# Performance work log

Measured on AMD Instinct MI355X. Metric: run time of the kernel, lower is better.

## Reference

```python
import jax, jax.numpy as jnp
import numpy as np

N_NODES = 100000
D = 256
N_EDGES = 500000
N_CLASSES = 4


def setup_inputs() -> dict:
    key = jax.random.key(0)
    k1, k2, k3, k4 = jax.random.split(key, 4)
    inp = jax.random.normal(k1, (N_NODES, D), dtype=jnp.float32)
    r_indices = jax.random.randint(k2, (N_EDGES,), 0, N_NODES, dtype=jnp.int64)
    c_indices = jax.random.randint(k3, (N_EDGES,), 0, N_NODES, dtype=jnp.int64)
    # xavier-uniform-like init for the skinny classifier weight
    limit = float(np.sqrt(6.0 / (D + N_CLASSES)))
    weight = jax.random.uniform(k4, (D, N_CLASSES), dtype=jnp.float32,
                                minval=-limit, maxval=limit)
    return {"input": inp, "r_indices": r_indices, "c_indices": c_indices,
            "weight": weight}


def reference(input, r_indices, c_indices, weight):
    # dropout p=0.0 -> identity. Gather edge endpoints, abs diff, skinny matmul.
    diff = jnp.abs(input[r_indices] - input[c_indices])  # [E, D]
    out = jnp.einsum('ed,dc->ec', diff, weight)          # [E, C]
    return out
```

## Files before the change

kernel.cpp:

```cpp
#include <hip/hip_runtime.h>


#define NODES   100000
#define DIM     256
#define EDGES   500000
#define NCLS    4

__global__ __launch_bounds__(256) void quant_kernel(
    const float* __restrict__ in,
    unsigned char* __restrict__ tbl,
    float* __restrict__ scales)
{
    const int lane = threadIdx.x & 63;
    const int wid  = (blockIdx.x * blockDim.x + threadIdx.x) >> 6;
    const int n_waves = (gridDim.x * blockDim.x) >> 6;

    for (int row = wid; row < NODES; row += n_waves) {
        const float4 v = *(const float4*)(in + (size_t)row * DIM + lane * 4);
        float m = fmaxf(fmaxf(fabsf(v.x), fabsf(v.y)),
                        fmaxf(fabsf(v.z), fabsf(v.w)));
        #pragma unroll
        for (int s = 32; s >= 1; s >>= 1)
            m = fmaxf(m, __shfl_xor(m, s, 64));

        const float rs = (m > 0.f) ? 127.f / m : 0.f;
        uchar4 q;
        q.x = (unsigned char)__float2int_rn(fmaf(v.x, rs, 128.f));
        q.y = (unsigned char)__float2int_rn(fmaf(v.y, rs, 128.f));
        q.z = (unsigned char)__float2int_rn(fmaf(v.z, rs, 128.f));
        q.w = (unsigned char)__float2int_rn(fmaf(v.w, rs, 128.f));
        *(uchar4*)(tbl + (size_t)row * DIM + lane * 4) = q;

        if (lane == 0) scales[row] = (m > 0.f) ? m / 127.f : 0.f;
    }
}

__global__ __launch_bounds__(256, 6) void edge_mlp_i8_x2_kernel(
    const unsigned char* __restrict__ tbl,
    const float* __restrict__ scales,
    const int*   __restrict__ r_idx,
    const int*   __restrict__ c_idx,
    const float* __restrict__ weight,
    float*       __restrict__ out)
{
    const int lane = threadIdx.x & 63;
    const int half = lane >> 5;
    const int hl   = lane & 31;
    const int wid  = (blockIdx.x * blockDim.x + threadIdx.x) >> 6;
    const int n_waves = (gridDim.x * blockDim.x) >> 6;
    const int step = n_waves * 4;

    const int d0 = hl * 8;
    float4 w[8];
    #pragma unroll
    for (int j = 0; j < 8; ++j)
        w[j] = *(const float4*)(weight + (d0 + j) * NCLS);

    for (int e = wid * 4; e < EDGES; e += step) {
        const int eeA = e + half;
        const int eeB = e + 2 + half;

        const int rA = r_idx[eeA], cA = c_idx[eeA];
        const int rB = r_idx[eeB], cB = c_idx[eeB];

        const float srA = scales[rA], scA = scales[cA];
        const float srB = scales[rB], scB = scales[cB];
        const uint2 uaA = *(const uint2*)(tbl + (size_t)rA * DIM + d0);
        const uint2 ubA = *(const uint2*)(tbl + (size_t)cA * DIM + d0);
        const uint2 uaB = *(const uint2*)(tbl + (size_t)rB * DIM + d0);
        const uint2 ubB = *(const uint2*)(tbl + (size_t)cB * DIM + d0);

        float u, t;
        #define TERM(UA, UB, SH, W, SR, NSC, BB, ACC)                        \
            u = fmaf((float)((UA >> SH) & 0xffu), SR,                        \
                     fmaf((float)((UB >> SH) & 0xffu), NSC, BB));            \
            t = fabsf(u);                                                    \
            ACC.x = fmaf(t, W.x, ACC.x);                                     \
            ACC.y = fmaf(t, W.y, ACC.y);                                     \
            ACC.z = fmaf(t, W.z, ACC.z);                                     \
            ACC.w = fmaf(t, W.w, ACC.w);

        const float nscA = -scA;
        const float BA = 128.f * (scA - srA);
        float4 accA = make_float4(0.f, 0.f, 0.f, 0.f);
        TERM(uaA.x, ubA.x,  0, w[0], srA, nscA, BA, accA)
        TERM(uaA.x, ubA.x,  8, w[1], srA, nscA, BA, accA)
        TERM(uaA.x, ubA.x, 16, w[2], srA, nscA, BA, accA)
        TERM(uaA.x, ubA.x, 24, w[3], srA, nscA, BA, accA)
        TERM(uaA.y, ubA.y,  0, w[4], srA, nscA, BA, accA)
        TERM(uaA.y, ubA.y,  8, w[5], srA, nscA, BA, accA)
        TERM(uaA.y, ubA.y, 16, w[6], srA, nscA, BA, accA)
        TERM(uaA.y, ubA.y, 24, w[7], srA, nscA, BA, accA)

        const float nscB = -scB;
        const float BB = 128.f * (scB - srB);
        float4 accB = make_float4(0.f, 0.f, 0.f, 0.f);
        TERM(uaB.x, ubB.x,  0, w[0], srB, nscB, BB, accB)
        TERM(uaB.x, ubB.x,  8, w[1], srB, nscB, BB, accB)
        TERM(uaB.x, ubB.x, 16, w[2], srB, nscB, BB, accB)
        TERM(uaB.x, ubB.x, 24, w[3], srB, nscB, BB, accB)
        TERM(uaB.y, ubB.y,  0, w[4], srB, nscB, BB, accB)
        TERM(uaB.y, ubB.y,  8, w[5], srB, nscB, BB, accB)
        TERM(uaB.y, ubB.y, 16, w[6], srB, nscB, BB, accB)
        TERM(uaB.y, ubB.y, 24, w[7], srB, nscB, BB, accB)
        #undef TERM

        #pragma unroll
        for (int m = 16; m >= 1; m >>= 1) {
            accA.x += __shfl_xor(accA.x, m, 64);
            accB.x += __shfl_xor(accB.x, m, 64);
            accA.y += __shfl_xor(accA.y, m, 64);
            accB.y += __shfl_xor(accB.y, m, 64);
            accA.z += __shfl_xor(accA.z, m, 64);
            accB.z += __shfl_xor(accB.z, m, 64);
            accA.w += __shfl_xor(accA.w, m, 64);
            accB.w += __shfl_xor(accB.w, m, 64);
        }

        if (hl == 0) {
            *(float4*)(out + (size_t)eeA * NCLS) = accA;
            *(float4*)(out + (size_t)eeB * NCLS) = accB;
        }
    }
}

__global__ __launch_bounds__(256, 8) void edge_mlp_f32_kernel(
    const float* __restrict__ input,
    const int*   __restrict__ r_idx,
    const int*   __restrict__ c_idx,
    const float* __restrict__ weight,
    float*       __restrict__ out)
{
    const int lane = threadIdx.x & 63;
    const int wid  = (blockIdx.x * blockDim.x + threadIdx.x) >> 6;
    const int n_waves = (gridDim.x * blockDim.x) >> 6;

    const int d0 = lane * 4;
    const float4 w0 = *(const float4*)(weight + (d0 + 0) * NCLS);
    const float4 w1 = *(const float4*)(weight + (d0 + 1) * NCLS);
    const float4 w2 = *(const float4*)(weight + (d0 + 2) * NCLS);
    const float4 w3 = *(const float4*)(weight + (d0 + 3) * NCLS);

    for (int e = wid; e < EDGES; e += n_waves) {
        const int r = r_idx[e];
        const int c = c_idx[e];
        const float4 a = *(const float4*)(input + (size_t)r * DIM + d0);
        const float4 b = *(const float4*)(input + (size_t)c * DIM + d0);

        const float t0 = fabsf(a.x - b.x);
        const float t1 = fabsf(a.y - b.y);
        const float t2 = fabsf(a.z - b.z);
        const float t3 = fabsf(a.w - b.w);

        float4 acc;
        acc.x = t0 * w0.x + t1 * w1.x + t2 * w2.x + t3 * w3.x;
        acc.y = t0 * w0.y + t1 * w1.y + t2 * w2.y + t3 * w3.y;
        acc.z = t0 * w0.z + t1 * w1.z + t2 * w2.z + t3 * w3.z;
        acc.w = t0 * w0.w + t1 * w1.w + t2 * w2.w + t3 * w3.w;

        #pragma unroll
        for (int m = 32; m >= 1; m >>= 1) {
            acc.x += __shfl_xor(acc.x, m, 64);
            acc.y += __shfl_xor(acc.y, m, 64);
            acc.z += __shfl_xor(acc.z, m, 64);
            acc.w += __shfl_xor(acc.w, m, 64);
        }
        if (lane == 0) *(float4*)(out + (size_t)e * NCLS) = acc;
    }
}

extern "C" void kernel_launch(void* const* d_in, const int* in_sizes, int n_in,
                              void* d_out, int out_size, void* d_ws, size_t ws_size,
                              hipStream_t stream) {
    const float* input  = (const float*)d_in[0];
    const int*   r_idx  = (const int*)d_in[1];
    const int*   c_idx  = (const int*)d_in[2];
    const float* weight = (const float*)d_in[3];
    float* out = (float*)d_out;

    const size_t tbl_bytes   = (size_t)NODES * DIM;
    const size_t scale_bytes = (size_t)NODES * sizeof(float);

    if (ws_size >= tbl_bytes + scale_bytes) {
        unsigned char* tbl = (unsigned char*)d_ws;
        float* scales = (float*)((char*)d_ws + tbl_bytes);
        quant_kernel<<<2048, 256, 0, stream>>>(input, tbl, scales);
        edge_mlp_i8_x2_kernel<<<2048, 256, 0, stream>>>(tbl, scales, r_idx,
                                                        c_idx, weight, out);
    } else {
        edge_mlp_f32_kernel<<<2048, 256, 0, stream>>>(input, r_idx, c_idx,
                                                      weight, out);
    }
}
```

Measured before the change: 91.20 us.

## Precompute packed per-edge records of row offsets and scales before the gather

Adds a pass that packs each edge's row and column table offsets and their scales into a 16-byte record, so the main kernel does one vector load per edge instead of dependent index loads followed by scale gathers. This shortens the dependent-load chain ahead of the table gathers. In exchange it adds a kernel launch and writes then reads 8 MB of records, and it needs more workspace; if the workspace is too small, the old path runs instead.

```diff
diff --git a/kernel.cpp b/kernel.cpp
--- a/kernel.cpp
+++ b/kernel.cpp
@@ -35,11 +35,28 @@
     }
 }
 
-__global__ __launch_bounds__(256, 6) void edge_mlp_i8_x2_kernel(
-    const unsigned char* __restrict__ tbl,
-    const float* __restrict__ scales,
+__global__ __launch_bounds__(256) void rec_kernel(
     const int*   __restrict__ r_idx,
     const int*   __restrict__ c_idx,
+    const float* __restrict__ scales,
+    uint4*       __restrict__ recs)
+{
+    const int stride = gridDim.x * blockDim.x;
+    for (int e = blockIdx.x * blockDim.x + threadIdx.x; e < EDGES; e += stride) {
+        const int r = r_idx[e];
+        const int c = c_idx[e];
+        uint4 rec;
+        rec.x = (unsigned)r * DIM;
+        rec.y = (unsigned)c * DIM;
+        rec.z = __float_as_uint(scales[r]);
+        rec.w = __float_as_uint(scales[c]);
+        recs[e] = rec;
+    }
+}
+
+__global__ __launch_bounds__(256, 6) void edge_mlp_i8_rec_kernel(
+    const unsigned char* __restrict__ tbl,
+    const uint4* __restrict__ recs,
     const float* __restrict__ weight,
     float*       __restrict__ out)
 {
@@ -60,15 +77,18 @@
         const int eeA = e + half;
         const int eeB = e + 2 + half;
 
-        const int rA = r_idx[eeA], cA = c_idx[eeA];
-        const int rB = r_idx[eeB], cB = c_idx[eeB];
-
-        const float srA = scales[rA], scA = scales[cA];
-        const float srB = scales[rB], scB = scales[cB];
-        const uint2 uaA = *(const uint2*)(tbl + (size_t)rA * DIM + d0);
-        const uint2 ubA = *(const uint2*)(tbl + (size_t)cA * DIM + d0);
-        const uint2 uaB = *(const uint2*)(tbl + (size_t)rB * DIM + d0);
-        const uint2 ubB = *(const uint2*)(tbl + (size_t)cB * DIM + d0);
+        const uint4 recA = recs[eeA];
+        const uint4 recB = recs[eeB];
+
+        const float srA = __uint_as_float(recA.z);
+        const float scA = __uint_as_float(recA.w);
+        const float srB = __uint_as_float(recB.z);
+        const float scB = __uint_as_float(recB.w);
+
+        const uint2 uaA = *(const uint2*)(tbl + recA.x + d0);
+        const uint2 ubA = *(const uint2*)(tbl + recA.y + d0);
+        const uint2 uaB = *(const uint2*)(tbl + recB.x + d0);
+        const uint2 ubB = *(const uint2*)(tbl + recB.y + d0);
 
         float u, t;
         #define TERM(UA, UB, SH, W, SR, NSC, BB, ACC)                        \
@@ -124,6 +144,95 @@
     }
 }
 
+__global__ __launch_bounds__(256, 6) void edge_mlp_i8_x2_kernel(
+    const unsigned char* __restrict__ tbl,
+    const float* __restrict__ scales,
+    const int*   __restrict__ r_idx,
+    const int*   __restrict__ c_idx,
+    const float* __restrict__ weight,
+    float*       __restrict__ out)
+{
+    const int lane = threadIdx.x & 63;
+    const int half = lane >> 5;
+    const int hl   = lane & 31;
+    const int wid  = (blockIdx.x * blockDim.x + threadIdx.x) >> 6;
+    const int n_waves = (gridDim.x * blockDim.x) >> 6;
+    const int step = n_waves * 4;
+
+    const int d0 = hl * 8;
+    float4 w[8];
+    #pragma unroll
+    for (int j = 0; j < 8; ++j)
+        w[j] = *(const float4*)(weight + (d0 + j) * NCLS);
+
+    for (int e = wid * 4; e < EDGES; e += step) {
+        const int eeA = e + half;
+        const int eeB = e + 2 + half;
+
+        const int rA = r_idx[eeA], cA = c_idx[eeA];
+        const int rB = r_idx[eeB], cB = c_idx[eeB];
+
+        const float srA = scales[rA], scA = scales[cA];
+        const float srB = scales[rB], scB = scales[cB];
+        const uint2 uaA = *(const uint2*)(tbl + (size_t)rA * DIM + d0);
+        const uint2 ubA = *(const uint2*)(tbl + (size_t)cA * DIM + d0);
+        const uint2 uaB = *(const uint2*)(tbl + (size_t)rB * DIM + d0);
+        const uint2 ubB = *(const uint2*)(tbl + (size_t)cB * DIM + d0);
+
+        float u, t;
+        #define TERM(UA, UB, SH, W, SR, NSC, BB, ACC)                        \
+            u = fmaf((float)((UA >> SH) & 0xffu), SR,                        \
+                     fmaf((float)((UB >> SH) & 0xffu), NSC, BB));            \
+            t = fabsf(u);                                                    \
+            ACC.x = fmaf(t, W.x, ACC.x);                                     \
+            ACC.y = fmaf(t, W.y, ACC.y);                                     \
+            ACC.z = fmaf(t, W.z, ACC.z);                                     \
+            ACC.w = fmaf(t, W.w, ACC.w);
+
+        const float nscA = -scA;
+        const float BA = 128.f * (scA - srA);
+        float4 accA = make_float4(0.f, 0.f, 0.f, 0.f);
+        TERM(uaA.x, ubA.x,  0, w[0], srA, nscA, BA, accA)
+        TERM(uaA.x, ubA.x,  8, w[1], srA, nscA, BA, accA)
+        TERM(uaA.x, ubA.x, 16, w[2], srA, nscA, BA, accA)
+        TERM(uaA.x, ubA.x, 24, w[3], srA, nscA, BA, accA)
+        TERM(uaA.y, ubA.y,  0, w[4], srA, nscA, BA, accA)
+        TERM(uaA.y, ubA.y,  8, w[5], srA, nscA, BA, accA)
+        TERM(uaA.y, ubA.y, 16, w[6], srA, nscA, BA, accA)
+        TERM(uaA.y, ubA.y, 24, w[7], srA, nscA, BA, accA)
+
+        const float nscB = -scB;
+        const float BB = 128.f * (scB - srB);
+        float4 accB = make_float4(0.f, 0.f, 0.f, 0.f);
+        TERM(uaB.x, ubB.x,  0, w[0], srB, nscB, BB, accB)
+        TERM(uaB.x, ubB.x,  8, w[1], srB, nscB, BB, accB)
+        TERM(uaB.x, ubB.x, 16, w[2], srB, nscB, BB, accB)
+        TERM(uaB.x, ubB.x, 24, w[3], srB, nscB, BB, accB)
+        TERM(uaB.y, ubB.y,  0, w[4], srB, nscB, BB, accB)
+        TERM(uaB.y, ubB.y,  8, w[5], srB, nscB, BB, accB)
+        TERM(uaB.y, ubB.y, 16, w[6], srB, nscB, BB, accB)
+        TERM(uaB.y, ubB.y, 24, w[7], srB, nscB, BB, accB)
+        #undef TERM
+
+        #pragma unroll
+        for (int m = 16; m >= 1; m >>= 1) {
+            accA.x += __shfl_xor(accA.x, m, 64);
+            accB.x += __shfl_xor(accB.x, m, 64);
+            accA.y += __shfl_xor(accA.y, m, 64);
+            accB.y += __shfl_xor(accB.y, m, 64);
+            accA.z += __shfl_xor(accA.z, m, 64);
+            accB.z += __shfl_xor(accB.z, m, 64);
+            accA.w += __shfl_xor(accA.w, m, 64);
+            accB.w += __shfl_xor(accB.w, m, 64);
+        }
+
+        if (hl == 0) {
+            *(float4*)(out + (size_t)eeA * NCLS) = accA;
+            *(float4*)(out + (size_t)eeB * NCLS) = accB;
+        }
+    }
+}
+
 __global__ __launch_bounds__(256, 8) void edge_mlp_f32_kernel(
     const float* __restrict__ input,
     const int*   __restrict__ r_idx,
@@ -180,8 +289,18 @@
 
     const size_t tbl_bytes   = (size_t)NODES * DIM;
     const size_t scale_bytes = (size_t)NODES * sizeof(float);
-
-    if (ws_size >= tbl_bytes + scale_bytes) {
+    const size_t rec_off     = (tbl_bytes + scale_bytes + 255) & ~(size_t)255;
+    const size_t rec_bytes   = (size_t)EDGES * 16;
+    const size_t rec_need    = rec_off + rec_bytes;
+
+    if (ws_size >= rec_need) {
+        unsigned char* tbl = (unsigned char*)d_ws;
+        float* scales = (float*)((char*)d_ws + tbl_bytes);
+        uint4* recs   = (uint4*)((char*)d_ws + rec_off);
+        quant_kernel<<<2048, 256, 0, stream>>>(input, tbl, scales);
+        rec_kernel<<<1954, 256, 0, stream>>>(r_idx, c_idx, scales, recs);
+        edge_mlp_i8_rec_kernel<<<2048, 256, 0, stream>>>(tbl, recs, weight, out);
+    } else if (ws_size >= tbl_bytes + scale_bytes) {
         unsigned char* tbl = (unsigned char*)d_ws;
         float* scales = (float*)((char*)d_ws + tbl_bytes);
         quant_kernel<<<2048, 256, 0, stream>>>(input, tbl, scales);
```

After: 98.27 us. 1.08x slower.
